# Optimization experiments

Measured on AMD Instinct MI355X. Metric: run time of the kernel, lower is better.

## Reference

```python
import jax, jax.numpy as jnp
import numpy as np

N_LABELS = 24
LABEL_DIM = 256
NEG = -10000.0


def setup_inputs() -> dict:
    key = jax.random.key(0)
    k1, k2 = jax.random.split(key, 2)
    B, L, DIM = 8, 512, 1024
    features = jax.random.normal(k1, (B, L, DIM), dtype=jnp.float32)
    mask = jnp.ones((B, L), dtype=bool)
    w_ff = jax.random.normal(k2, (N_LABELS * LABEL_DIM * 2, DIM), dtype=jnp.float32) * 0.02
    b_ff = jnp.zeros((N_LABELS * LABEL_DIM * 2,), dtype=jnp.float32)
    bias = jnp.zeros((N_LABELS,), dtype=jnp.float32)
    return {"features": features, "mask": mask, "w_ff": w_ff, "b_ff": b_ff, "bias": bias}


def reference(features, mask, w_ff, b_ff, bias):
    B, L, _ = features.shape
    # ff -> relu -> split into start/end features per label
    x = jax.nn.relu(jnp.einsum('bld,od->blo', features, w_ff) + b_ff)  # [B,L,n_labels*label_dim*2]
    x = x.reshape(B, L, N_LABELS, LABEL_DIM, 2)
    start_f = x[..., 0]  # [B,L,n_labels,label_dim]
    end_f = x[..., 1]
    # biaffine pairwise span scores: [B, n_labels, start, end]
    scores = jnp.einsum('bsld,beld->blse', start_f, end_f) + bias[None, :, None, None]
    # remove_nan branch: replace inf/nan with -10000
    scores = jnp.where(jnp.isinf(scores) | jnp.isnan(scores), NEG, scores)
    # triangular + padding mask over (start, end)
    triu = jnp.triu(jnp.ones((L, L), dtype=bool))  # start <= end
    spans_mask = triu[None] & mask[:, :, None] & mask[:, None, :]  # [B,L,L]
    masked_scores = jnp.where(spans_mask[:, None, :, :], scores, NEG)
    return scores, masked_scores
```

## Files before the change

kernel.cpp:

```cpp
#include <hip/hip_runtime.h>
#include <hip/hip_bf16.h>

#define NLAB  24
#define LDIM  256
#define LSEQ  512
#define DDIM  1024
#define NOUT  12288
#define NEGV  (-10000.0f)
#define MOFF  50331648L

typedef __attribute__((ext_vector_type(8))) short short8;
typedef __attribute__((ext_vector_type(4))) float f32x4;
typedef unsigned short u16;
typedef unsigned int   u32;

typedef const __attribute__((address_space(1))) void gvoid_t;
typedef __attribute__((address_space(3))) void lvoid_t;

__device__ __forceinline__ u16 f2bf(float f) {
  u32 u = __builtin_bit_cast(u32, f);
  u32 r = u + 0x7FFFu + ((u >> 16) & 1u);
  return (u16)(r >> 16);
}

__device__ __forceinline__ void g2l16(const u16* g, u16* l) {
  __builtin_amdgcn_global_load_lds((gvoid_t*)g, (lvoid_t*)l, 16, 0, 0);
}

__global__ void cvt_bf16_kernel(const float* __restrict__ feat,
                                const float* __restrict__ wff,
                                u16* __restrict__ fA, u16* __restrict__ fB) {
  const long NA = 4194304L;
  const long NB = 12582912L;
  const long NQ = (NA + NB) / 4;
  long stride = (long)gridDim.x * blockDim.x;
  for (long i = (long)blockIdx.x * blockDim.x + threadIdx.x; i < NQ; i += stride) {
    long e = i * 4;
    const float* s; u16* d;
    if (e < NA) { s = feat + e;        d = fA + e; }
    else        { s = wff + (e - NA);  d = fB + (e - NA); }
    float4 v = *reinterpret_cast<const float4*>(s);
    ushort4 o;
    o.x = f2bf(v.x); o.y = f2bf(v.y); o.z = f2bf(v.z); o.w = f2bf(v.w);
    *reinterpret_cast<ushort4*>(d) = o;
  }
}

__global__ __launch_bounds__(256)
void ff_gemm_kernel(const u16* __restrict__ A, const u16* __restrict__ B,
                    const float* __restrict__ bff,
                    u16* __restrict__ sf, u16* __restrict__ ef) {
  __shared__ __align__(16) u16 As[128 * 32];
  __shared__ __align__(16) u16 Bs[128 * 32];
  const int tid  = threadIdx.x;
  const int lane = tid & 63;
  const int wv   = tid >> 6;
  const int wm   = wv >> 1, wn = wv & 1;
  const int tm = blockIdx.x / (NOUT / 128);
  const int tn = blockIdx.x % (NOUT / 128);
  const int rowA0 = tm * 128, rowB0 = tn * 128;

  const int srow = tid >> 2;
  const int scol = (tid & 3) * 8;
  const u16* ga = A + (long)(rowA0 + srow) * DDIM + scol;
  const u16* gb = B + (long)(rowB0 + srow) * DDIM + scol;
  u16* la = As + tid * 8;
  u16* lb = Bs + tid * 8;

  f32x4 acc[4][4] = {};
  const int lr = lane & 15;
  const int lk = (lane >> 4) * 8;

  for (int k0 = 0; k0 < DDIM; k0 += 32) {
    g2l16(ga + k0,             la);
    g2l16(ga + k0 + 64 * DDIM, la + 2048);
    g2l16(gb + k0,             lb);
    g2l16(gb + k0 + 64 * DDIM, lb + 2048);
    __syncthreads();
    short8 af[4], bfr[4];
#pragma unroll
    for (int f = 0; f < 4; ++f) {
      af[f]  = *reinterpret_cast<const short8*>(As + (wm * 64 + f * 16 + lr) * 32 + lk);
      bfr[f] = *reinterpret_cast<const short8*>(Bs + (wn * 64 + f * 16 + lr) * 32 + lk);
    }
#pragma unroll
    for (int i = 0; i < 4; ++i)
#pragma unroll
      for (int j = 0; j < 4; ++j)
        acc[i][j] = __builtin_amdgcn_mfma_f32_16x16x32_bf16(af[i], bfr[j], acc[i][j], 0, 0, 0);
    __syncthreads();
  }

  const int r0 = (lane >> 4) * 4;
#pragma unroll
  for (int j = 0; j < 4; ++j) {
    const int o = rowB0 + wn * 64 + j * 16 + lr;
    const float bv = bff[o];
    const int label = o >> 9, d = (o >> 1) & 255, se = o & 1;
    u16* dst0 = se ? ef : sf;
#pragma unroll
    for (int i = 0; i < 4; ++i) {
#pragma unroll
      for (int r = 0; r < 4; ++r) {
        const int m = rowA0 + wm * 64 + i * 16 + r0 + r;
        const int b = m >> 9, ll = m & 511;
        float v = acc[i][j][r] + bv;
        v = v > 0.f ? v : 0.f;
        dst0[((long)(b * NLAB + label) * LSEQ + ll) * LDIM + d] = f2bf(v);
      }
    }
  }
}

__global__ __launch_bounds__(256)
void biaffine_kernel(const u16* __restrict__ sf, const u16* __restrict__ ef,
                     const float* __restrict__ bias, const int* __restrict__ mask,
                     float* __restrict__ out) {
  __shared__ __align__(16) u16 As[128 * 32];
  __shared__ __align__(16) u16 Bs[128 * 32];
  const int tid = threadIdx.x, lane = tid & 63, wv = tid >> 6;
  const int wm = wv >> 1, wn = wv & 1;
  const int bl   = blockIdx.x >> 4;
  const int tile = blockIdx.x & 15;
  const int tm = tile >> 2, tn = tile & 3;
  const int b = bl / NLAB, label = bl - b * NLAB;
  const u16* Abase = sf + (long)bl * LSEQ * LDIM;
  const u16* Bbase = ef + (long)bl * LSEQ * LDIM;
  const int rowA0 = tm * 128, rowB0 = tn * 128;

  const int srow = tid >> 2, scol = (tid & 3) * 8;
  const u16* ga = Abase + (long)(rowA0 + srow) * LDIM + scol;
  const u16* gb = Bbase + (long)(rowB0 + srow) * LDIM + scol;
  u16* la = As + tid * 8;
  u16* lb = Bs + tid * 8;

  f32x4 acc[4][4] = {};
  const int lr = lane & 15, lk = (lane >> 4) * 8;

  for (int k0 = 0; k0 < LDIM; k0 += 32) {
    g2l16(ga + k0,             la);
    g2l16(ga + k0 + 64 * LDIM, la + 2048);
    g2l16(gb + k0,             lb);
    g2l16(gb + k0 + 64 * LDIM, lb + 2048);
    __syncthreads();
    short8 af[4], bfr[4];
#pragma unroll
    for (int f = 0; f < 4; ++f) {
      af[f]  = *reinterpret_cast<const short8*>(As + (wm * 64 + f * 16 + lr) * 32 + lk);
      bfr[f] = *reinterpret_cast<const short8*>(Bs + (wn * 64 + f * 16 + lr) * 32 + lk);
    }
#pragma unroll
    for (int i = 0; i < 4; ++i)
#pragma unroll
      for (int j = 0; j < 4; ++j)
        acc[i][j] = __builtin_amdgcn_mfma_f32_16x16x32_bf16(af[i], bfr[j], acc[i][j], 0, 0, 0);
    __syncthreads();
  }

  const float bv = bias[label];
  const int r0 = (lane >> 4) * 4;
  const long obase0 = (long)bl * LSEQ * LSEQ;
#pragma unroll
  for (int i = 0; i < 4; ++i) {
#pragma unroll
    for (int r = 0; r < 4; ++r) {
      const int s = rowA0 + wm * 64 + i * 16 + r0 + r;
      const bool ms = (mask[b * LSEQ + s] != 0);
#pragma unroll
      for (int j = 0; j < 4; ++j) {
        const int e = rowB0 + wn * 64 + j * 16 + lr;
        float v = acc[i][j][r] + bv;
        u32 bits = __builtin_bit_cast(u32, v);
        if ((bits & 0x7F800000u) == 0x7F800000u) v = NEGV;
        const long idx = obase0 + (long)s * LSEQ + e;
        out[idx] = v;
        const bool keep = (s <= e) && ms && (mask[b * LSEQ + e] != 0);
        out[MOFF + idx] = keep ? v : NEGV;
      }
    }
  }
}

extern "C" void kernel_launch(void* const* d_in, const int* in_sizes, int n_in,
                              void* d_out, int out_size, void* d_ws, size_t ws_size,
                              hipStream_t stream) {
  const float* feat = (const float*)d_in[0];
  const int*   mask = (const int*)d_in[1];
  const float* wff  = (const float*)d_in[2];
  const float* bff  = (const float*)d_in[3];
  const float* bias = (const float*)d_in[4];
  float* out = (float*)d_out;

  u16* fA = (u16*)d_ws;
  u16* fB = fA + 4194304L;
  u16* sf = fB + 12582912L;
  u16* ef = sf + 25165824L;

  cvt_bf16_kernel<<<2048, 256, 0, stream>>>(feat, wff, fA, fB);
  ff_gemm_kernel<<<dim3(32 * (NOUT / 128)), 256, 0, stream>>>(fA, fB, bff, sf, ef);
  biaffine_kernel<<<dim3(192 * 16), 256, 0, stream>>>(sf, ef, bias, mask, out);
}
```

Baseline: 312.9 us.

## Use 256x256 double-buffered swizzled tiles for both GEMM kernels

Both GEMMs move from 128x128 tiles with 256 threads and K-step 32 to 256x256 tiles with 512 threads, K-step 64, and double-buffered LDS staging so the next tile's loads overlap the current MFMAs. LDS rows are XOR-swizzled to avoid bank conflicts. The ff GEMM permutes B rows so each lane's output columns line up with the start/end interleave. Block IDs are remapped across groups of 8, and s_setprio raises priority around the MFMA bursts. The goal is more operand reuse and fewer barrier stalls, at the cost of 128 KB of LDS per block and higher register pressure with 128 accumulator floats per lane.

```diff
diff --git a/kernel.cpp b/kernel.cpp
--- a/kernel.cpp
+++ b/kernel.cpp
@@ -46,136 +46,170 @@
   }
 }
 
-__global__ __launch_bounds__(256)
-void ff_gemm_kernel(const u16* __restrict__ A, const u16* __restrict__ B,
-                    const float* __restrict__ bff,
-                    u16* __restrict__ sf, u16* __restrict__ ef) {
-  __shared__ __align__(16) u16 As[128 * 32];
-  __shared__ __align__(16) u16 Bs[128 * 32];
-  const int tid  = threadIdx.x;
-  const int lane = tid & 63;
-  const int wv   = tid >> 6;
-  const int wm   = wv >> 1, wn = wv & 1;
-  const int tm = blockIdx.x / (NOUT / 128);
-  const int tn = blockIdx.x % (NOUT / 128);
-  const int rowA0 = tm * 128, rowB0 = tn * 128;
-
-  const int srow = tid >> 2;
-  const int scol = (tid & 3) * 8;
-  const u16* ga = A + (long)(rowA0 + srow) * DDIM + scol;
-  const u16* gb = B + (long)(rowB0 + srow) * DDIM + scol;
-  u16* la = As + tid * 8;
-  u16* lb = Bs + tid * 8;
-
-  f32x4 acc[4][4] = {};
-  const int lr = lane & 15;
-  const int lk = (lane >> 4) * 8;
-
-  for (int k0 = 0; k0 < DDIM; k0 += 32) {
-    g2l16(ga + k0,             la);
-    g2l16(ga + k0 + 64 * DDIM, la + 2048);
-    g2l16(gb + k0,             lb);
-    g2l16(gb + k0 + 64 * DDIM, lb + 2048);
+template<int LDK, bool PERM>
+__device__ __forceinline__ void stage_tile(const u16* __restrict__ gbase, int row0,
+                                           int k0, u16* lbuf, int t) {
+#pragma unroll
+  for (int l = 0; l < 4; ++l) {
+    const int rt = l * 64 + (t >> 3);
+    const int ce = ((t & 7) ^ (rt & 7)) << 3;
+    int gr = rt;
+    if (PERM) gr = (rt & ~31) | ((rt & 15) << 1) | ((rt >> 4) & 1);
+    g2l16(gbase + (long)(row0 + gr) * LDK + k0 + ce, lbuf + (l * 512 + t) * 8);
+  }
+}
+
+#define FRAG_OFF(r, ks, hi) (((r) * 64 + (ks) * 32 + (hi) * 8) ^ (((r) & 7) << 3))
+
+__global__ __launch_bounds__(512, 2)
+void ff_gemm256(const u16* __restrict__ A, const u16* __restrict__ B,
+                const float* __restrict__ bff,
+                u16* __restrict__ sf, u16* __restrict__ ef) {
+  __shared__ __align__(16) u16 lds[2][2][16384];
+  const int tid = threadIdx.x, lane = tid & 63, wv = tid >> 6;
+  const int wm = wv >> 2, wn = wv & 3;
+  const int lr = lane & 15, hi = lane >> 4;
+
+  const int bid = blockIdx.x;
+  const int wg  = (bid & 7) * 96 + (bid >> 3);
+  const int tm  = wg & 15, tn = wg >> 4;
+  const int rowA0 = tm * 256, rowB0 = tn * 256;
+
+  f32x4 acc[8][4] = {};
+
+  stage_tile<DDIM, false>(A, rowA0, 0, lds[0][0], tid);
+  stage_tile<DDIM, true >(B, rowB0, 0, lds[0][1], tid);
+  __syncthreads();
+
+  int buf = 0;
+  for (int t = 0; t < 16; ++t) {
+    if (t < 15) {
+      stage_tile<DDIM, false>(A, rowA0, (t + 1) * 64, lds[buf ^ 1][0], tid);
+      stage_tile<DDIM, true >(B, rowB0, (t + 1) * 64, lds[buf ^ 1][1], tid);
+    }
+    const u16* La = lds[buf][0];
+    const u16* Lb = lds[buf][1];
+#pragma unroll
+    for (int ks = 0; ks < 2; ++ks) {
+      short8 af[8], bfr[4];
+#pragma unroll
+      for (int i = 0; i < 8; ++i) {
+        const int r = wm * 128 + i * 16 + lr;
+        af[i] = *reinterpret_cast<const short8*>(La + FRAG_OFF(r, ks, hi));
+      }
+#pragma unroll
+      for (int j = 0; j < 4; ++j) {
+        const int r = wn * 64 + j * 16 + lr;
+        bfr[j] = *reinterpret_cast<const short8*>(Lb + FRAG_OFF(r, ks, hi));
+      }
+      __builtin_amdgcn_s_setprio(1);
+#pragma unroll
+      for (int i = 0; i < 8; ++i)
+#pragma unroll
+        for (int j = 0; j < 4; ++j)
+          acc[i][j] = __builtin_amdgcn_mfma_f32_16x16x32_bf16(af[i], bfr[j], acc[i][j], 0, 0, 0);
+      __builtin_amdgcn_s_setprio(0);
+    }
     __syncthreads();
-    short8 af[4], bfr[4];
-#pragma unroll
-    for (int f = 0; f < 4; ++f) {
-      af[f]  = *reinterpret_cast<const short8*>(As + (wm * 64 + f * 16 + lr) * 32 + lk);
-      bfr[f] = *reinterpret_cast<const short8*>(Bs + (wn * 64 + f * 16 + lr) * 32 + lk);
-    }
-#pragma unroll
-    for (int i = 0; i < 4; ++i)
-#pragma unroll
-      for (int j = 0; j < 4; ++j)
-        acc[i][j] = __builtin_amdgcn_mfma_f32_16x16x32_bf16(af[i], bfr[j], acc[i][j], 0, 0, 0);
-    __syncthreads();
-  }
-
-  const int r0 = (lane >> 4) * 4;
+    buf ^= 1;
+  }
+
 #pragma unroll
   for (int j = 0; j < 4; ++j) {
-    const int o = rowB0 + wn * 64 + j * 16 + lr;
+    const int cblk = wn * 64 + j * 16;
+    const int o = rowB0 + (cblk & ~31) + 2 * lr + ((cblk >> 4) & 1);
     const float bv = bff[o];
     const int label = o >> 9, d = (o >> 1) & 255, se = o & 1;
-    u16* dst0 = se ? ef : sf;
-#pragma unroll
-    for (int i = 0; i < 4; ++i) {
+    u16* dst = se ? ef : sf;
+#pragma unroll
+    for (int i = 0; i < 8; ++i) {
 #pragma unroll
       for (int r = 0; r < 4; ++r) {
-        const int m = rowA0 + wm * 64 + i * 16 + r0 + r;
+        const int m = rowA0 + wm * 128 + i * 16 + hi * 4 + r;
         const int b = m >> 9, ll = m & 511;
         float v = acc[i][j][r] + bv;
         v = v > 0.f ? v : 0.f;
-        dst0[((long)(b * NLAB + label) * LSEQ + ll) * LDIM + d] = f2bf(v);
-      }
-    }
-  }
-}
-
-__global__ __launch_bounds__(256)
-void biaffine_kernel(const u16* __restrict__ sf, const u16* __restrict__ ef,
-                     const float* __restrict__ bias, const int* __restrict__ mask,
-                     float* __restrict__ out) {
-  __shared__ __align__(16) u16 As[128 * 32];
-  __shared__ __align__(16) u16 Bs[128 * 32];
+        dst[((long)(b * NLAB + label) * LSEQ + ll) * LDIM + d] = f2bf(v);
+      }
+    }
+  }
+}
+
+__global__ __launch_bounds__(512, 2)
+void biaffine256(const u16* __restrict__ sf, const u16* __restrict__ ef,
+                 const float* __restrict__ bias, const int* __restrict__ mask,
+                 float* __restrict__ out) {
+  __shared__ __align__(16) u16 lds[2][2][16384];
   const int tid = threadIdx.x, lane = tid & 63, wv = tid >> 6;
-  const int wm = wv >> 1, wn = wv & 1;
-  const int bl   = blockIdx.x >> 4;
-  const int tile = blockIdx.x & 15;
-  const int tm = tile >> 2, tn = tile & 3;
+  const int wm = wv >> 2, wn = wv & 3;
+  const int lr = lane & 15, hi = lane >> 4;
+
+  const int bid = blockIdx.x;
+  const int wg  = (bid & 7) * 96 + (bid >> 3);
+  const int bl  = wg >> 2, tile = wg & 3;
+  const int tm  = tile >> 1, tn = tile & 1;
   const int b = bl / NLAB, label = bl - b * NLAB;
-  const u16* Abase = sf + (long)bl * LSEQ * LDIM;
-  const u16* Bbase = ef + (long)bl * LSEQ * LDIM;
-  const int rowA0 = tm * 128, rowB0 = tn * 128;
-
-  const int srow = tid >> 2, scol = (tid & 3) * 8;
-  const u16* ga = Abase + (long)(rowA0 + srow) * LDIM + scol;
-  const u16* gb = Bbase + (long)(rowB0 + srow) * LDIM + scol;
-  u16* la = As + tid * 8;
-  u16* lb = Bs + tid * 8;
-
-  f32x4 acc[4][4] = {};
-  const int lr = lane & 15, lk = (lane >> 4) * 8;
-
-  for (int k0 = 0; k0 < LDIM; k0 += 32) {
-    g2l16(ga + k0,             la);
-    g2l16(ga + k0 + 64 * LDIM, la + 2048);
-    g2l16(gb + k0,             lb);
-    g2l16(gb + k0 + 64 * LDIM, lb + 2048);
+  const u16* Ab = sf + (long)bl * LSEQ * LDIM;
+  const u16* Bb = ef + (long)bl * LSEQ * LDIM;
+  const int rowA0 = tm * 256, rowB0 = tn * 256;
+
+  f32x4 acc[8][4] = {};
+
+  stage_tile<LDIM, false>(Ab, rowA0, 0, lds[0][0], tid);
+  stage_tile<LDIM, false>(Bb, rowB0, 0, lds[0][1], tid);
+  __syncthreads();
+
+  int buf = 0;
+  for (int t = 0; t < 4; ++t) {
+    if (t < 3) {
+      stage_tile<LDIM, false>(Ab, rowA0, (t + 1) * 64, lds[buf ^ 1][0], tid);
+      stage_tile<LDIM, false>(Bb, rowB0, (t + 1) * 64, lds[buf ^ 1][1], tid);
+    }
+    const u16* La = lds[buf][0];
+    const u16* Lb = lds[buf][1];
+#pragma unroll
+    for (int ks = 0; ks < 2; ++ks) {
+      short8 af[8], bfr[4];
+#pragma unroll
+      for (int i = 0; i < 8; ++i) {
+        const int r = wm * 128 + i * 16 + lr;
+        af[i] = *reinterpret_cast<const short8*>(La + FRAG_OFF(r, ks, hi));
+      }
+#pragma unroll
+      for (int j = 0; j < 4; ++j) {
+        const int r = wn * 64 + j * 16 + lr;
+        bfr[j] = *reinterpret_cast<const short8*>(Lb + FRAG_OFF(r, ks, hi));
+      }
+      __builtin_amdgcn_s_setprio(1);
+#pragma unroll
+      for (int i = 0; i < 8; ++i)
+#pragma unroll
+        for (int j = 0; j < 4; ++j)
+          acc[i][j] = __builtin_amdgcn_mfma_f32_16x16x32_bf16(af[i], bfr[j], acc[i][j], 0, 0, 0);
+      __builtin_amdgcn_s_setprio(0);
+    }
     __syncthreads();
-    short8 af[4], bfr[4];
-#pragma unroll
-    for (int f = 0; f < 4; ++f) {
-      af[f]  = *reinterpret_cast<const short8*>(As + (wm * 64 + f * 16 + lr) * 32 + lk);
-      bfr[f] = *reinterpret_cast<const short8*>(Bs + (wn * 64 + f * 16 + lr) * 32 + lk);
-    }
-#pragma unroll
-    for (int i = 0; i < 4; ++i)
-#pragma unroll
-      for (int j = 0; j < 4; ++j)
-        acc[i][j] = __builtin_amdgcn_mfma_f32_16x16x32_bf16(af[i], bfr[j], acc[i][j], 0, 0, 0);
-    __syncthreads();
+    buf ^= 1;
   }
 
   const float bv = bias[label];
-  const int r0 = (lane >> 4) * 4;
-  const long obase0 = (long)bl * LSEQ * LSEQ;
-#pragma unroll
-  for (int i = 0; i < 4; ++i) {
+  const long obase = (long)bl * LSEQ * LSEQ;
+#pragma unroll
+  for (int i = 0; i < 8; ++i) {
 #pragma unroll
     for (int r = 0; r < 4; ++r) {
-      const int s = rowA0 + wm * 64 + i * 16 + r0 + r;
+      const int s = rowA0 + wm * 128 + i * 16 + hi * 4 + r;
       const bool ms = (mask[b * LSEQ + s] != 0);
+      const long rbase = obase + (long)s * LSEQ;
 #pragma unroll
       for (int j = 0; j < 4; ++j) {
         const int e = rowB0 + wn * 64 + j * 16 + lr;
         float v = acc[i][j][r] + bv;
         u32 bits = __builtin_bit_cast(u32, v);
         if ((bits & 0x7F800000u) == 0x7F800000u) v = NEGV;
-        const long idx = obase0 + (long)s * LSEQ + e;
-        out[idx] = v;
+        out[rbase + e] = v;
         const bool keep = (s <= e) && ms && (mask[b * LSEQ + e] != 0);
-        out[MOFF + idx] = keep ? v : NEGV;
+        out[MOFF + rbase + e] = keep ? v : NEGV;
       }
     }
   }
@@ -197,6 +231,6 @@
   u16* ef = sf + 25165824L;
 
   cvt_bf16_kernel<<<2048, 256, 0, stream>>>(feat, wff, fA, fB);
-  ff_gemm_kernel<<<dim3(32 * (NOUT / 128)), 256, 0, stream>>>(fA, fB, bff, sf, ef);
-  biaffine_kernel<<<dim3(192 * 16), 256, 0, stream>>>(sf, ef, bias, mask, out);
-}
+  ff_gemm256<<<768, 512, 0, stream>>>(fA, fB, bff, sf, ef);
+  biaffine256<<<768, 512, 0, stream>>>(sf, ef, bias, mask, out);
+}
```

After: 254.0 us. -18.8%, faster.
